# Kernel tuning notes

Hardware: AMD Instinct MI355X
Metric: run time of the kernel (lower is better)

The kernel has to match this reference:

```python
import jax, jax.numpy as jnp
import numpy as np

L = 32      # num_layer
N_ORD = 64  # order_of_a_LTImodel
U = 64      # u_size
Y = 64      # y_size
T = 8192    # sequence length
SCALE = 0.05  # keep block-bidiagonal A spectrally stable over 8192 steps


def setup_inputs() -> dict:
    key = jax.random.key(0)
    k_u, k_a, k_b0, k_bl, k_c = jax.random.split(key, 5)
    inp = {
        "input": jax.random.normal(k_u, (T, U), dtype=jnp.float32),
        # per-layer A_i weights (diagonal blocks)
        "A_stack": jax.random.normal(k_a, (L, N_ORD, N_ORD), dtype=jnp.float32) * SCALE,
        # layer-0 B (maps u -> state)
        "B0": jax.random.normal(k_b0, (N_ORD, U), dtype=jnp.float32) * SCALE,
        # layer i>=1 B weights (sub-diagonal coupling blocks)
        "B_lower": jax.random.normal(k_bl, (L - 1, N_ORD, N_ORD), dtype=jnp.float32) * SCALE,
        # per-layer C_i weights, concatenated along columns in forward
        "C_stack": jax.random.normal(k_c, (L, Y, N_ORD), dtype=jnp.float32),
        # D is frozen zeros (feedthrough=False)
        "D_w": jnp.zeros((Y, U), dtype=jnp.float32),
    }
    return inp


def _assemble(A_stack, B0, B_lower, C_stack):
    l, n, _ = A_stack.shape
    S = l * n
    A = jnp.zeros((S, S), A_stack.dtype)
    for i in range(l):  # fixed small structural loop
        A = A.at[i * n:(i + 1) * n, i * n:(i + 1) * n].set(A_stack[i])
    for i in range(1, l):
        A = A.at[i * n:(i + 1) * n, (i - 1) * n:i * n].set(B_lower[i - 1])
    B = jnp.concatenate([B0, jnp.zeros((S - n, B0.shape[1]), B0.dtype)], axis=0)
    # torch.cat([C_i], dim=1): [Y, L*n]
    C = jnp.transpose(C_stack, (1, 0, 2)).reshape(C_stack.shape[1], S)
    return A, B, C


def reference(input, A_stack, B0, B_lower, C_stack, D_w):
    A, B, C = _assemble(A_stack, B0, B_lower, C_stack)
    S = A.shape[0]
    x0 = jnp.zeros((S,), input.dtype)

    def step(x, u):
        y = C @ x + D_w @ u      # output BEFORE state update (y_t uses x_t)
        x_next = A @ x + B @ u
        return x_next, y

    _, ys = jax.lax.scan(step, x0, input)
    return ys  # [T, Y]
```

## Files before the change

### kernel.cpp

```cpp
#include <hip/hip_runtime.h>


#define LYR 32
#define NO  64
#define TSEQ 8192
#define PAD 32
#define PR2 (TSEQ+PAD)
#define PB2 ((size_t)PR2*NO)
#define KQ  2048

typedef _Float16 h16;
typedef _Float16 h16x8 __attribute__((ext_vector_type(8)));
typedef float    f32x4 __attribute__((ext_vector_type(4)));

#define MFMA16(a,b,c) __builtin_amdgcn_mfma_f32_16x16x32_f16((a),(b),(c),0,0,0)

__global__ __launch_bounds__(256) void prep_build(
    const float* __restrict__ u, const float* __restrict__ B0,
    const float* __restrict__ Bl, const float* __restrict__ Cst,
    const float* __restrict__ Ast,
    h16* __restrict__ xq, h16* __restrict__ ccast,
    h16* __restrict__ SN, h16* __restrict__ ST,
    h16* __restrict__ ktq, float* __restrict__ Dacc)
{
    __shared__ __align__(16) h16   Ah[64*72];
    __shared__ __align__(16) h16   kT[64*72];
    __shared__ __align__(16) float kf[64*68];
    const int tid = threadIdx.x;

    if (blockIdx.x < 32) {
        const int layer = blockIdx.x;
        const bool wantST = (layer & 3) == 0;
        const float* k0 = (layer == 0) ? B0 : (Bl + (size_t)(layer-1)*4096);
        const float* Aw = Ast + (size_t)layer*4096;
        for (int e8 = tid; e8 < 512; e8 += 256) {
            int n = e8 >> 3, m0 = (e8 & 7) << 3;
            f32x4 a0 = *(const f32x4*)&Aw[n*64 + m0];
            f32x4 a1 = *(const f32x4*)&Aw[n*64 + m0 + 4];
            h16 ah[8];
            #pragma unroll
            for (int t = 0; t < 4; t++) { ah[t] = (h16)a0[t]; ah[4+t] = (h16)a1[t]; }
            *(int4*)&Ah[n*72 + m0] = *(int4*)&ah[0];
            f32x4 b0 = *(const f32x4*)&k0[n*64 + m0];
            f32x4 b1 = *(const f32x4*)&k0[n*64 + m0 + 4];
            *(f32x4*)&kf[n*68 + m0]     = b0;
            *(f32x4*)&kf[n*68 + m0 + 4] = b1;
        }
        __syncthreads();

        const int wv = tid >> 6, lane = tid & 63, r = lane & 15, q = lane >> 4;
        const h16x8 a0 = *(const h16x8*)&Ah[(wv*16 + r)*72 + q*8];
        const h16x8 a1 = *(const h16x8*)&Ah[(wv*16 + r)*72 + 32 + q*8];

        for (int j = 0; j < 16; j++) {
            if (j > 0) {
                f32x4 acc[4] = {};
                #pragma unroll
                for (int c = 0; c < 4; c++) {
                    h16x8 b0 = *(const h16x8*)&kT[(c*16 + r)*72 + q*8];
                    h16x8 b1 = *(const h16x8*)&kT[(c*16 + r)*72 + 32 + q*8];
                    acc[c] = MFMA16(a0, b0, acc[c]);
                    acc[c] = MFMA16(a1, b1, acc[c]);
                }
                #pragma unroll
                for (int c = 0; c < 4; c++)
                    #pragma unroll
                    for (int g4 = 0; g4 < 4; g4++)
                        kf[(wv*16 + q*4 + g4)*68 + c*16 + r] = acc[c][g4];
                __syncthreads();
            }
            size_t base = (size_t)(layer*16 + j)*4096;
            for (int e8 = tid; e8 < 512; e8 += 256) {
                int n = e8 >> 3, m0 = (e8 & 7) << 3;
                f32x4 v0 = *(const f32x4*)&kf[n*68 + m0];
                f32x4 v1 = *(const f32x4*)&kf[n*68 + m0 + 4];
                h16 o[8];
                #pragma unroll
                for (int t = 0; t < 4; t++) { o[t] = (h16)v0[t]; o[4+t] = (h16)v1[t]; }
                if (!wantST)
                    *(int4*)&SN[base + (size_t)n*64 + m0] = *(int4*)&o[0];
                #pragma unroll
                for (int t = 0; t < 8; t++)
                    kT[(m0 + t)*72 + n] = o[t];
                if (wantST) {
                    h16 o2[8];
                    #pragma unroll
                    for (int t = 0; t < 8; t++) o2[t] = (h16)kf[(m0 + t)*68 + n];
                    *(int4*)&ST[base + (size_t)n*64 + m0] = *(int4*)&o2[0];
                }
            }
            __syncthreads();
        }
        return;
    }

    const int s1 = 256;
    const int s2 = 65536;
    const int s3 = 1792;
    const int s4 = 16384;
    const int s5 = 131072;
    const int s6 = 262144;
    const int total = s1+s2+s3+s4+s5+s6;
    const int4 z4 = make_int4(0,0,0,0);
    for (int e0 = (blockIdx.x - 32)*256 + tid; e0 < total; e0 += 512*256) {
        int e = e0;
        if (e < s1) { *(int4*)&xq[e*8] = z4; continue; }
        e -= s1;
        if (e < s2) {
            int el = e*8;
            f32x4 f0 = *(const f32x4*)&u[el];
            f32x4 f1 = *(const f32x4*)&u[el+4];
            h16 ov[8];
            #pragma unroll
            for (int j = 0; j < 4; j++) { ov[j] = (h16)f0[j]; ov[4+j] = (h16)f1[j]; }
            *(int4*)&xq[PAD*NO + el] = *(int4*)&ov[0];
            continue;
        }
        e -= s2;
        if (e < s3) {
            int b = e >> 8, off = (e & 255)*8;
            *(int4*)&xq[(size_t)(b+1)*PB2 + off] = z4;
            continue;
        }
        e -= s3;
        if (e < s4) {
            int el = e*8;
            f32x4 f0 = *(const f32x4*)&Cst[el];
            f32x4 f1 = *(const f32x4*)&Cst[el+4];
            h16 ov[8];
            #pragma unroll
            for (int j = 0; j < 4; j++) { ov[j] = (h16)f0[j]; ov[4+j] = (h16)f1[j]; }
            *(int4*)&ccast[el] = *(int4*)&ov[0];
            continue;
        }
        e -= s4;
        if (e < s5) { *(int4*)&ktq[e*8] = z4; continue; }
        e -= s5;
        *(int4*)&Dacc[e*4] = z4;
    }
}

__device__ __forceinline__ void comp_mm(const h16* __restrict__ X,
                                        const h16* __restrict__ Y,
                                        int wv, int r, int q, f32x4 acc[4])
{
    h16x8 a0 = *(const h16x8*)(X + (wv*16 + r)*64 + q*8);
    h16x8 a1 = *(const h16x8*)(X + (wv*16 + r)*64 + 32 + q*8);
    #pragma unroll
    for (int c = 0; c < 4; c++) {
        h16x8 b0 = *(const h16x8*)(Y + (c*16 + r)*64 + q*8);
        h16x8 b1 = *(const h16x8*)(Y + (c*16 + r)*64 + 32 + q*8);
        acc[c] = MFMA16(a0, b0, acc[c]);
        acc[c] = MFMA16(a1, b1, acc[c]);
    }
}

__global__ __launch_bounds__(256) void compose2(
    const h16* __restrict__ SN, const h16* __restrict__ ST,
    const h16* __restrict__ cc, h16* __restrict__ P2T,
    float* __restrict__ Dacc)
{
    const int tid = threadIdx.x, wv = tid>>6, lane = tid&63, r = lane&15, q = lane>>4;
    f32x4 acc[4] = {};
    int bid = blockIdx.x;
    if (bid < 248) {
        int g = bid / 31, m2 = bid % 31;
        int j0 = m2 > 15 ? m2 - 15 : 0;
        int j1 = m2 < 15 ? m2 : 15;
        const h16* X = SN + ((size_t)(4*g+1)*16 + j0)*4096;
        const h16* Y = ST + ((size_t)(4*g)*16 + (m2 - j0))*4096;
        for (int it = 0; it <= j1 - j0; ++it) {
            comp_mm(X, Y, wv, r, q, acc);
            X += 4096; Y -= 4096;
        }
        h16* o = P2T + ((size_t)g*31 + m2)*4096;
        #pragma unroll
        for (int c = 0; c < 4; c++)
            #pragma unroll
            for (int g4 = 0; g4 < 4; g4++)
                o[(c*16+r)*64 + wv*16 + q*4 + g4] = (h16)acc[c][g4];
    } else {
        int idx = bid - 248, g = idx >> 4, j = idx & 15;
        comp_mm(cc + (size_t)(4*g)*4096, ST + ((size_t)(4*g)*16 + j)*4096, wv, r, q, acc);
        float* Dd = Dacc + ((size_t)g*32 + j)*4096;
        #pragma unroll
        for (int c = 0; c < 4; c++)
            #pragma unroll
            for (int g4 = 0; g4 < 4; g4++)
                atomicAdd(&Dd[(wv*16 + q*4 + g4)*64 + c*16 + r], acc[c][g4]);
    }
}

__global__ __launch_bounds__(256) void compose3(
    const h16* __restrict__ SN, const h16* __restrict__ cc,
    const h16* __restrict__ P2T, h16* __restrict__ P3T,
    float* __restrict__ Dacc)
{
    const int tid = threadIdx.x, wv = tid>>6, lane = tid&63, r = lane&15, q = lane>>4;
    f32x4 acc[4] = {};
    int bid = blockIdx.x;
    if (bid < 240) {
        int g = bid / 30, m3 = bid % 30;
        int j1 = m3 < 15 ? m3 : 15;
        const h16* X = SN + ((size_t)(4*g+2)*16)*4096;
        const h16* Y = P2T + ((size_t)g*31 + m3)*4096;
        for (int it = 0; it <= j1; ++it) {
            comp_mm(X, Y, wv, r, q, acc);
            X += 4096; Y -= 4096;
        }
        h16* o = P3T + ((size_t)g*30 + m3)*4096;
        #pragma unroll
        for (int c = 0; c < 4; c++)
            #pragma unroll
            for (int g4 = 0; g4 < 4; g4++)
                o[(c*16+r)*64 + wv*16 + q*4 + g4] = (h16)acc[c][g4];
    } else {
        int idx = bid - 240, g = idx / 31, m2 = idx % 31;
        comp_mm(cc + (size_t)(4*g+1)*4096, P2T + ((size_t)g*31 + m2)*4096, wv, r, q, acc);
        float* Dd = Dacc + ((size_t)g*32 + m2 + 1)*4096;
        #pragma unroll
        for (int c = 0; c < 4; c++)
            #pragma unroll
            for (int g4 = 0; g4 < 4; g4++)
                atomicAdd(&Dd[(wv*16 + q*4 + g4)*64 + c*16 + r], acc[c][g4]);
    }
}

__global__ __launch_bounds__(256) void compose4(
    const h16* __restrict__ SN, const h16* __restrict__ cc,
    const h16* __restrict__ P3T, h16* __restrict__ ktq,
    float* __restrict__ Dacc)
{
    __shared__ h16 ldsT[64*72];
    const int tid = threadIdx.x, wv = tid>>6, lane = tid&63, r = lane&15, q = lane>>4;
    f32x4 acc[4] = {};
    int bid = blockIdx.x;
    if (bid < 232) {
        int g = bid / 29, m4 = bid % 29;
        int j1 = m4 < 15 ? m4 : 15;
        const h16* X = SN + ((size_t)(4*g+3)*16)*4096;
        const h16* Y = P3T + ((size_t)g*30 + m4)*4096;
        for (int it = 0; it <= j1; ++it) {
            comp_mm(X, Y, wv, r, q, acc);
            X += 4096; Y -= 4096;
        }
        h16* kq = ktq + (size_t)g*131072 + (size_t)(28 - m4)*64;
        #pragma unroll
        for (int c = 0; c < 4; c++)
            #pragma unroll
            for (int g4 = 0; g4 < 4; g4++) {
                h16 v = (h16)acc[c][g4];
                kq[(size_t)(wv*16 + q*4 + g4)*KQ + c*16 + r] = v;
                ldsT[(c*16+r)*72 + wv*16 + q*4 + g4] = v;
            }
        __syncthreads();
        f32x4 acc2[4] = {};
        const h16* Xc = cc + (size_t)(4*g+3)*4096;
        h16x8 a0 = *(const h16x8*)(Xc + (wv*16 + r)*64 + q*8);
        h16x8 a1 = *(const h16x8*)(Xc + (wv*16 + r)*64 + 32 + q*8);
        #pragma unroll
        for (int c = 0; c < 4; c++) {
            h16x8 b0 = *(const h16x8*)(&ldsT[(c*16+r)*72 + q*8]);
            h16x8 b1 = *(const h16x8*)(&ldsT[(c*16+r)*72 + 32 + q*8]);
            acc2[c] = MFMA16(a0, b0, acc2[c]);
            acc2[c] = MFMA16(a1, b1, acc2[c]);
        }
        float* Dd = Dacc + ((size_t)g*32 + m4 + 3)*4096;
        #pragma unroll
        for (int c = 0; c < 4; c++)
            #pragma unroll
            for (int g4 = 0; g4 < 4; g4++)
                atomicAdd(&Dd[(wv*16 + q*4 + g4)*64 + c*16 + r], acc2[c][g4]);
    } else {
        int idx = bid - 232, g = idx / 30, m3 = idx % 30;
        comp_mm(cc + (size_t)(4*g+2)*4096, P3T + ((size_t)g*30 + m3)*4096, wv, r, q, acc);
        float* Dd = Dacc + ((size_t)g*32 + m3 + 2)*4096;
        #pragma unroll
        for (int c = 0; c < 4; c++)
            #pragma unroll
            for (int g4 = 0; g4 < 4; g4++)
                atomicAdd(&Dd[(wv*16 + q*4 + g4)*64 + c*16 + r], acc[c][g4]);
    }
}

__global__ __launch_bounds__(256) void castD(const float* __restrict__ Dacc,
                                             h16* __restrict__ ktd)
{
    const int total4 = 8*32*4096/4;
    for (int idx4 = blockIdx.x*256 + threadIdx.x; idx4 < total4; idx4 += 256*256) {
        int idx = idx4 << 2;
        int gdo = idx >> 12;
        int g = gdo >> 5, dd = gdo & 31;
        int rem = idx & 4095;
        int y = rem >> 6, m = rem & 63;
        f32x4 f = *(const f32x4*)&Dacc[idx];
        h16 o4[4];
        #pragma unroll
        for (int t = 0; t < 4; t++) o4[t] = (h16)f[t];
        *(int2*)&ktd[(size_t)g*131072 + (size_t)y*KQ + (31 - dd)*64 + m] = *(int2*)&o4[0];
    }
}

template<int WRST>
__global__ __launch_bounds__(512) void stage(
    const h16* __restrict__ pin, h16* __restrict__ pout,
    const h16* __restrict__ ktqg, const h16* __restrict__ ktdg,
    float* __restrict__ out, int first)
{
    __shared__ __align__(16) h16   win[96*72];
    __shared__ __align__(16) float red[4*32*68];
    const int tid = threadIdx.x;
    const size_t t0 = (size_t)blockIdx.x * 64;

    for (int e = tid; e < 96*8; e += 512) {
        int rr = e >> 3, cc = e & 7;
        *(int4*)&win[rr*72 + cc*8] = *(const int4*)&pin[(t0 + rr)*64 + cc*8];
    }
    __syncthreads();

    const int wv = tid >> 6, lane = tid & 63, r = lane & 15, q = lane >> 4;
    const int half = wv >> 2, kq = wv & 3;
    const bool active = WRST || (half == 1);
    f32x4 acc[2][2][4] = {};
    if (active) {
        const h16* kb = half ? ktdg : ktqg;
        const h16* abase = &win[(r + kq*8)*72 + q*8];
        const h16* bbase = kb + (size_t)r*KQ + kq*512 + q*8;
#define LDA(st, s, ls) (*(const h16x8*)(abase + ((st)*32 + (s)*16 + ((ls)>>1))*72 + ((ls)&1)*32))
#define LDB(c, ls) (*(const h16x8*)(bbase + (size_t)(c)*(16*KQ) + (ls)*32))
        h16x8 a[2][2][2], b[2][4];
        #pragma unroll
        for (int sl = 0; sl < 2; sl++) {
            #pragma unroll
            for (int st = 0; st < 2; st++)
                #pragma unroll
                for (int s = 0; s < 2; s++) a[sl][st][s] = LDA(st, s, sl);
            #pragma unroll
            for (int c = 0; c < 4; c++) b[sl][c] = LDB(c, sl);
        }
        #pragma unroll
        for (int ls = 0; ls < 16; ls++) {
            h16x8 ca[2][2], cb[4];
            #pragma unroll
            for (int st = 0; st < 2; st++)
                #pragma unroll
                for (int s = 0; s < 2; s++) ca[st][s] = a[ls&1][st][s];
            #pragma unroll
            for (int c = 0; c < 4; c++) cb[c] = b[ls&1][c];
            if (ls < 14) {
                #pragma unroll
                for (int st = 0; st < 2; st++)
                    #pragma unroll
                    for (int s = 0; s < 2; s++) a[ls&1][st][s] = LDA(st, s, ls+2);
                #pragma unroll
                for (int c = 0; c < 4; c++) b[ls&1][c] = LDB(c, ls+2);
            }
            #pragma unroll
            for (int st = 0; st < 2; st++)
                #pragma unroll
                for (int s = 0; s < 2; s++)
                    #pragma unroll
                    for (int c = 0; c < 4; c++)
                        acc[st][s][c] = MFMA16(ca[st][s], cb[c], acc[st][s][c]);
        }
#undef LDA
#undef LDB
    }

    const int rh = half * (2*32*68);
    #pragma unroll
    for (int st = 0; st < 2; st++) {
        __syncthreads();
        if (active && kq >= 2) {
            float* myred = red + rh + (kq-2)*(32*68);
            #pragma unroll
            for (int s2 = 0; s2 < 2; s2++)
                #pragma unroll
                for (int c = 0; c < 4; c++)
                    #pragma unroll
                    for (int g4 = 0; g4 < 4; g4++)
                        myred[(s2*16 + q*4 + g4)*68 + c*16 + r] = acc[st][s2][c][g4];
        }
        __syncthreads();
        if (active && kq < 2) {
            float* myred = red + rh + kq*(32*68);
            #pragma unroll
            for (int s2 = 0; s2 < 2; s2++)
                #pragma unroll
                for (int c = 0; c < 4; c++)
                    #pragma unroll
                    for (int g4 = 0; g4 < 4; g4++)
                        myred[(s2*16 + q*4 + g4)*68 + c*16 + r] += acc[st][s2][c][g4];
        }
        __syncthreads();
        if (WRST && tid < 256) {
            int orow = tid >> 3, cb2 = (tid & 7) << 3;
            f32x4 u0 = *(const f32x4*)&red[orow*68 + cb2];
            f32x4 u1 = *(const f32x4*)&red[orow*68 + cb2 + 4];
            f32x4 v0 = *(const f32x4*)&red[32*68 + orow*68 + cb2];
            f32x4 v1 = *(const f32x4*)&red[32*68 + orow*68 + cb2 + 4];
            u0 += v0; u1 += v1;
            h16 ov[8];
            #pragma unroll
            for (int j = 0; j < 4; j++) { ov[j] = (h16)u0[j]; ov[4+j] = (h16)u1[j]; }
            *(int4*)&pout[(PAD + t0 + st*32 + orow)*64 + cb2] = *(int4*)&ov[0];
        }
        if (tid >= 256) {
            int t2 = tid - 256;
            int orow = t2 >> 3, cb2 = (t2 & 7) << 3;
            const float* base = red + 2*32*68;
            f32x4 u0 = *(const f32x4*)&base[orow*68 + cb2];
            f32x4 u1 = *(const f32x4*)&base[orow*68 + cb2 + 4];
            f32x4 v0 = *(const f32x4*)&base[32*68 + orow*68 + cb2];
            f32x4 v1 = *(const f32x4*)&base[32*68 + orow*68 + cb2 + 4];
            u0 += v0; u1 += v1;
            float* op = out + (t0 + st*32 + orow)*64 + cb2;
            if (first) {
                *(f32x4*)op = u0; *(f32x4*)(op+4) = u1;
            } else {
                f32x4 o0 = *(f32x4*)op, o1 = *(f32x4*)(op+4);
                o0 += u0; o1 += u1;
                *(f32x4*)op = o0; *(f32x4*)(op+4) = o1;
            }
        }
    }
}

extern "C" void kernel_launch(void* const* d_in, const int* in_sizes, int n_in,
                              void* d_out, int out_size, void* d_ws, size_t ws_size,
                              hipStream_t stream)
{
    const float* u   = (const float*)d_in[0];
    const float* Ast = (const float*)d_in[1];
    const float* B0  = (const float*)d_in[2];
    const float* Bl  = (const float*)d_in[3];
    const float* Cst = (const float*)d_in[4];
    float* out = (float*)d_out;
    (void)in_sizes; (void)n_in; (void)out_size; (void)ws_size;

    char* ws = (char*)d_ws;
    h16*   xq    = (h16*)ws;
    h16*   ccast = (h16*)(ws + 8421376);
    h16*   SN    = (h16*)(ws + 8683520);
    h16*   ST    = (h16*)(ws + 12877824);
    h16*   P2T   = (h16*)(ws + 17072128);
    h16*   P3T   = (h16*)(ws + 19103744);
    h16*   ktq   = (h16*)(ws + 21069824);
    h16*   ktd   = (h16*)(ws + 23166976);
    float* Dacc  = (float*)(ws + 25264128);

    prep_build<<<544, 256, 0, stream>>>(u, B0, Bl, Cst, Ast, xq, ccast, SN, ST, ktq, Dacc);
    compose2<<<376, 256, 0, stream>>>(SN, ST, ccast, P2T, Dacc);
    compose3<<<488, 256, 0, stream>>>(SN, ccast, P2T, P3T, Dacc);
    compose4<<<472, 256, 0, stream>>>(SN, ccast, P3T, ktq, Dacc);
    castD<<<256, 256, 0, stream>>>(Dacc, ktd);
    for (int g = 0; g < 7; g++) {
        stage<1><<<TSEQ/64, 512, 0, stream>>>(xq + (size_t)g*PB2, xq + (size_t)(g+1)*PB2,
                                              ktq + (size_t)g*131072, ktd + (size_t)g*131072,
                                              out, g == 0);
    }
    stage<0><<<TSEQ/64, 512, 0, stream>>>(xq + (size_t)7*PB2, xq,
                                          ktq + (size_t)7*131072, ktd + (size_t)7*131072,
                                          out, 0);
}
```

Baseline: 303.0 us.

## Compose layer-group kernels to 8-layer groups, halving sequential stage launches

Adds a compose5 pass that convolves pairs of 4-layer impulse-response blocks into 8-layer kernels (ktq8/ktd8). The sequential stage chain across the sequence then runs 4 launches instead of 8. Padding and window sizes are adjusted for the longer composed kernels. The goal is to cut serialized stage passes and reloads of intermediate state, at the cost of extra composition work and more fp16 rounding through the deeper products.

```diff
diff --git a/kernel.cpp b/kernel.cpp
--- a/kernel.cpp
+++ b/kernel.cpp
@@ -1,19 +1,20 @@
 #include <hip/hip_runtime.h>
 
 
-#define LYR 32
-#define NO  64
+#define NO   64
 #define TSEQ 8192
-#define PAD 32
-#define PR2 (TSEQ+PAD)
-#define PB2 ((size_t)PR2*NO)
-#define KQ  2048
+#define PAD8 40
+#define PRX  8240
+#define PBX  ((size_t)PRX*NO)
+#define KQ   2048
 
 typedef _Float16 h16;
 typedef _Float16 h16x8 __attribute__((ext_vector_type(8)));
 typedef float    f32x4 __attribute__((ext_vector_type(4)));
 
 #define MFMA16(a,b,c) __builtin_amdgcn_mfma_f32_16x16x32_f16((a),(b),(c),0,0,0)
+#define IMAX(a,b) ((a)>(b)?(a):(b))
+#define IMIN(a,b) ((a)<(b)?(a):(b))
 
 __global__ __launch_bounds__(256) void prep_build(
     const float* __restrict__ u, const float* __restrict__ B0,
@@ -21,7 +22,7 @@
     const float* __restrict__ Ast,
     h16* __restrict__ xq, h16* __restrict__ ccast,
     h16* __restrict__ SN, h16* __restrict__ ST,
-    h16* __restrict__ ktq, float* __restrict__ Dacc)
+    float* __restrict__ Dacc)
 {
     __shared__ __align__(16) h16   Ah[64*72];
     __shared__ __align__(16) h16   kT[64*72];
@@ -41,17 +42,13 @@
             #pragma unroll
             for (int t = 0; t < 4; t++) { ah[t] = (h16)a0[t]; ah[4+t] = (h16)a1[t]; }
             *(int4*)&Ah[n*72 + m0] = *(int4*)&ah[0];
-            f32x4 b0 = *(const f32x4*)&k0[n*64 + m0];
-            f32x4 b1 = *(const f32x4*)&k0[n*64 + m0 + 4];
-            *(f32x4*)&kf[n*68 + m0]     = b0;
-            *(f32x4*)&kf[n*68 + m0 + 4] = b1;
+            *(f32x4*)&kf[n*68 + m0]     = *(const f32x4*)&k0[n*64 + m0];
+            *(f32x4*)&kf[n*68 + m0 + 4] = *(const f32x4*)&k0[n*64 + m0 + 4];
         }
         __syncthreads();
-
         const int wv = tid >> 6, lane = tid & 63, r = lane & 15, q = lane >> 4;
         const h16x8 a0 = *(const h16x8*)&Ah[(wv*16 + r)*72 + q*8];
         const h16x8 a1 = *(const h16x8*)&Ah[(wv*16 + r)*72 + 32 + q*8];
-
         for (int j = 0; j < 16; j++) {
             if (j > 0) {
                 f32x4 acc[4] = {};
@@ -94,13 +91,12 @@
         return;
     }
 
-    const int s1 = 256;
+    const int s1 = 320;
     const int s2 = 65536;
-    const int s3 = 1792;
+    const int s3 = 960;
     const int s4 = 16384;
-    const int s5 = 131072;
     const int s6 = 262144;
-    const int total = s1+s2+s3+s4+s5+s6;
+    const int total = s1+s2+s3+s4+s6;
     const int4 z4 = make_int4(0,0,0,0);
     for (int e0 = (blockIdx.x - 32)*256 + tid; e0 < total; e0 += 512*256) {
         int e = e0;
@@ -113,13 +109,13 @@
             h16 ov[8];
             #pragma unroll
             for (int j = 0; j < 4; j++) { ov[j] = (h16)f0[j]; ov[4+j] = (h16)f1[j]; }
-            *(int4*)&xq[PAD*NO + el] = *(int4*)&ov[0];
+            *(int4*)&xq[PAD8*NO + el] = *(int4*)&ov[0];
             continue;
         }
         e -= s2;
         if (e < s3) {
-            int b = e >> 8, off = (e & 255)*8;
-            *(int4*)&xq[(size_t)(b+1)*PB2 + off] = z4;
+            int b = e / 320, off = (e % 320)*8;
+            *(int4*)&xq[(size_t)(b+1)*PBX + off] = z4;
             continue;
         }
         e -= s3;
@@ -134,8 +130,6 @@
             continue;
         }
         e -= s4;
-        if (e < s5) { *(int4*)&ktq[e*8] = z4; continue; }
-        e -= s5;
         *(int4*)&Dacc[e*4] = z4;
     }
 }
@@ -154,6 +148,30 @@
         acc[c] = MFMA16(a1, b1, acc[c]);
     }
 }
+__device__ __forceinline__ void conv_loop(const h16* X, const h16* Y, int n,
+                                          int wv, int r, int q, f32x4 acc[4])
+{
+    for (int it = 0; it < n; ++it) {
+        comp_mm(X, Y, wv, r, q, acc);
+        X += 4096; Y -= 4096;
+    }
+}
+__device__ __forceinline__ void write_N(h16* o, int wv, int r, int q, const f32x4 acc[4])
+{
+    #pragma unroll
+    for (int c = 0; c < 4; c++)
+        #pragma unroll
+        for (int g4 = 0; g4 < 4; g4++)
+            o[(size_t)(wv*16 + q*4 + g4)*64 + c*16 + r] = (h16)acc[c][g4];
+}
+__device__ __forceinline__ void write_T(h16* o, int wv, int r, int q, const f32x4 acc[4])
+{
+    #pragma unroll
+    for (int c = 0; c < 4; c++)
+        #pragma unroll
+        for (int g4 = 0; g4 < 4; g4++)
+            o[(size_t)(c*16 + r)*64 + wv*16 + q*4 + g4] = (h16)acc[c][g4];
+}
 
 __global__ __launch_bounds__(256) void compose2(
     const h16* __restrict__ SN, const h16* __restrict__ ST,
@@ -165,24 +183,15 @@
     int bid = blockIdx.x;
     if (bid < 248) {
         int g = bid / 31, m2 = bid % 31;
-        int j0 = m2 > 15 ? m2 - 15 : 0;
-        int j1 = m2 < 15 ? m2 : 15;
-        const h16* X = SN + ((size_t)(4*g+1)*16 + j0)*4096;
-        const h16* Y = ST + ((size_t)(4*g)*16 + (m2 - j0))*4096;
-        for (int it = 0; it <= j1 - j0; ++it) {
-            comp_mm(X, Y, wv, r, q, acc);
-            X += 4096; Y -= 4096;
-        }
-        h16* o = P2T + ((size_t)g*31 + m2)*4096;
-        #pragma unroll
-        for (int c = 0; c < 4; c++)
-            #pragma unroll
-            for (int g4 = 0; g4 < 4; g4++)
-                o[(c*16+r)*64 + wv*16 + q*4 + g4] = (h16)acc[c][g4];
+        int j0 = IMAX(0, m2 - 15);
+        int j1 = IMIN(15, m2);
+        conv_loop(SN + ((size_t)((4*g+1)*16) + j0)*4096,
+                  ST + ((size_t)((4*g)*16) + (m2 - j0))*4096, j1-j0+1, wv, r, q, acc);
+        write_T(P2T + ((size_t)(g*31 + m2))*4096, wv, r, q, acc);
     } else {
         int idx = bid - 248, g = idx >> 4, j = idx & 15;
-        comp_mm(cc + (size_t)(4*g)*4096, ST + ((size_t)(4*g)*16 + j)*4096, wv, r, q, acc);
-        float* Dd = Dacc + ((size_t)g*32 + j)*4096;
+        comp_mm(cc + (size_t)(4*g)*4096, ST + ((size_t)((4*g)*16) + j)*4096, wv, r, q, acc);
+        float* Dd = Dacc + ((size_t)(g*32 + j))*4096;
         #pragma unroll
         for (int c = 0; c < 4; c++)
             #pragma unroll
@@ -201,23 +210,14 @@
     int bid = blockIdx.x;
     if (bid < 240) {
         int g = bid / 30, m3 = bid % 30;
-        int j1 = m3 < 15 ? m3 : 15;
-        const h16* X = SN + ((size_t)(4*g+2)*16)*4096;
-        const h16* Y = P2T + ((size_t)g*31 + m3)*4096;
-        for (int it = 0; it <= j1; ++it) {
-            comp_mm(X, Y, wv, r, q, acc);
-            X += 4096; Y -= 4096;
-        }
-        h16* o = P3T + ((size_t)g*30 + m3)*4096;
-        #pragma unroll
-        for (int c = 0; c < 4; c++)
-            #pragma unroll
-            for (int g4 = 0; g4 < 4; g4++)
-                o[(c*16+r)*64 + wv*16 + q*4 + g4] = (h16)acc[c][g4];
+        int j1 = IMIN(15, m3);
+        conv_loop(SN + ((size_t)((4*g+2)*16))*4096,
+                  P2T + ((size_t)(g*31 + m3))*4096, j1+1, wv, r, q, acc);
+        write_T(P3T + ((size_t)(g*30 + m3))*4096, wv, r, q, acc);
     } else {
         int idx = bid - 240, g = idx / 31, m2 = idx % 31;
-        comp_mm(cc + (size_t)(4*g+1)*4096, P2T + ((size_t)g*31 + m2)*4096, wv, r, q, acc);
-        float* Dd = Dacc + ((size_t)g*32 + m2 + 1)*4096;
+        comp_mm(cc + (size_t)(4*g+1)*4096, P2T + ((size_t)(g*31 + m2))*4096, wv, r, q, acc);
+        float* Dd = Dacc + ((size_t)(g*32 + m2 + 1))*4096;
         #pragma unroll
         for (int c = 0; c < 4; c++)
             #pragma unroll
@@ -228,7 +228,8 @@
 
 __global__ __launch_bounds__(256) void compose4(
     const h16* __restrict__ SN, const h16* __restrict__ cc,
-    const h16* __restrict__ P3T, h16* __restrict__ ktq,
+    const h16* __restrict__ P3T,
+    h16* __restrict__ P4N, h16* __restrict__ P4T,
     float* __restrict__ Dacc)
 {
     __shared__ h16 ldsT[64*72];
@@ -237,22 +238,16 @@
     int bid = blockIdx.x;
     if (bid < 232) {
         int g = bid / 29, m4 = bid % 29;
-        int j1 = m4 < 15 ? m4 : 15;
-        const h16* X = SN + ((size_t)(4*g+3)*16)*4096;
-        const h16* Y = P3T + ((size_t)g*30 + m4)*4096;
-        for (int it = 0; it <= j1; ++it) {
-            comp_mm(X, Y, wv, r, q, acc);
-            X += 4096; Y -= 4096;
-        }
-        h16* kq = ktq + (size_t)g*131072 + (size_t)(28 - m4)*64;
-        #pragma unroll
-        for (int c = 0; c < 4; c++)
-            #pragma unroll
-            for (int g4 = 0; g4 < 4; g4++) {
-                h16 v = (h16)acc[c][g4];
-                kq[(size_t)(wv*16 + q*4 + g4)*KQ + c*16 + r] = v;
-                ldsT[(c*16+r)*72 + wv*16 + q*4 + g4] = v;
-            }
+        int j1 = IMIN(15, m4);
+        conv_loop(SN + ((size_t)((4*g+3)*16))*4096,
+                  P3T + ((size_t)(g*30 + m4))*4096, j1+1, wv, r, q, acc);
+        write_N(P4N + ((size_t)(g*29 + m4))*4096, wv, r, q, acc);
+        write_T(P4T + ((size_t)(g*29 + m4))*4096, wv, r, q, acc);
+        #pragma unroll
+        for (int c = 0; c < 4; c++)
+            #pragma unroll
+            for (int g4 = 0; g4 < 4; g4++)
+                ldsT[(c*16+r)*72 + wv*16 + q*4 + g4] = (h16)acc[c][g4];
         __syncthreads();
         f32x4 acc2[4] = {};
         const h16* Xc = cc + (size_t)(4*g+3)*4096;
@@ -265,7 +260,7 @@
             acc2[c] = MFMA16(a0, b0, acc2[c]);
             acc2[c] = MFMA16(a1, b1, acc2[c]);
         }
-        float* Dd = Dacc + ((size_t)g*32 + m4 + 3)*4096;
+        float* Dd = Dacc + ((size_t)(g*32 + m4 + 3))*4096;
         #pragma unroll
         for (int c = 0; c < 4; c++)
             #pragma unroll
@@ -273,8 +268,8 @@
                 atomicAdd(&Dd[(wv*16 + q*4 + g4)*64 + c*16 + r], acc2[c][g4]);
     } else {
         int idx = bid - 232, g = idx / 30, m3 = idx % 30;
-        comp_mm(cc + (size_t)(4*g+2)*4096, P3T + ((size_t)g*30 + m3)*4096, wv, r, q, acc);
-        float* Dd = Dacc + ((size_t)g*32 + m3 + 2)*4096;
+        comp_mm(cc + (size_t)(4*g+2)*4096, P3T + ((size_t)(g*30 + m3))*4096, wv, r, q, acc);
+        float* Dd = Dacc + ((size_t)(g*32 + m3 + 2))*4096;
         #pragma unroll
         for (int c = 0; c < 4; c++)
             #pragma unroll
@@ -284,37 +279,73 @@
 }
 
 __global__ __launch_bounds__(256) void castD(const float* __restrict__ Dacc,
-                                             h16* __restrict__ ktd)
+                                             h16* __restrict__ D4N)
 {
     const int total4 = 8*32*4096/4;
     for (int idx4 = blockIdx.x*256 + threadIdx.x; idx4 < total4; idx4 += 256*256) {
         int idx = idx4 << 2;
-        int gdo = idx >> 12;
-        int g = gdo >> 5, dd = gdo & 31;
-        int rem = idx & 4095;
-        int y = rem >> 6, m = rem & 63;
         f32x4 f = *(const f32x4*)&Dacc[idx];
         h16 o4[4];
         #pragma unroll
         for (int t = 0; t < 4; t++) o4[t] = (h16)f[t];
-        *(int2*)&ktd[(size_t)g*131072 + (size_t)y*KQ + (31 - dd)*64 + m] = *(int2*)&o4[0];
+        *(int2*)&D4N[idx] = *(int2*)&o4[0];
+    }
+}
+
+__global__ __launch_bounds__(256) void compose5(
+    const h16* __restrict__ P4N, const h16* __restrict__ P4T,
+    const h16* __restrict__ D4N, const float* __restrict__ D4F,
+    h16* __restrict__ ktq8, h16* __restrict__ ktd8)
+{
+    const int tid = threadIdx.x, wv = tid>>6, lane = tid&63, r = lane&15, q = lane>>4;
+    f32x4 acc[4] = {};
+    int bid = blockIdx.x;
+    if (bid < 128) {
+        int o = bid >> 5, m = bid & 31, D = m + 8;
+        int j0 = IMAX(4, D-32), j1 = IMIN(32, D-4);
+        conv_loop(P4N + ((size_t)((2*o+1)*29) + (j0-4))*4096,
+                  P4T + ((size_t)((2*o)*29) + (D-j0-4))*4096, j1-j0+1, wv, r, q, acc);
+        h16* kq = ktq8 + (size_t)o*131072 + (size_t)(39 - D)*64;
+        #pragma unroll
+        for (int c = 0; c < 4; c++)
+            #pragma unroll
+            for (int g4 = 0; g4 < 4; g4++)
+                kq[(size_t)(wv*16 + q*4 + g4)*KQ + c*16 + r] = (h16)acc[c][g4];
+    } else {
+        int idx = bid - 128, o = idx >> 5, m = idx & 31, D = m + 1;
+        int n = D - 4;
+        if (n > 0)
+            conv_loop(D4N + ((size_t)((2*o+1)*32))*4096,
+                      P4T + ((size_t)((2*o)*29) + (D-1-4))*4096, n, wv, r, q, acc);
+        const float* DF = D4F + ((size_t)((2*o)*32 + D-1))*4096;
+        #pragma unroll
+        for (int c = 0; c < 4; c++)
+            #pragma unroll
+            for (int g4 = 0; g4 < 4; g4++)
+                acc[c][g4] += DF[(size_t)(wv*16 + q*4 + g4)*64 + c*16 + r];
+        h16* kd = ktd8 + (size_t)o*131072 + (size_t)(32 - D)*64;
+        #pragma unroll
+        for (int c = 0; c < 4; c++)
+            #pragma unroll
+            for (int g4 = 0; g4 < 4; g4++)
+                kd[(size_t)(wv*16 + q*4 + g4)*KQ + c*16 + r] = (h16)acc[c][g4];
     }
 }
 
 template<int WRST>
-__global__ __launch_bounds__(512) void stage(
+__global__ __launch_bounds__(512) void stage8(
     const h16* __restrict__ pin, h16* __restrict__ pout,
     const h16* __restrict__ ktqg, const h16* __restrict__ ktdg,
     float* __restrict__ out, int first)
 {
-    __shared__ __align__(16) h16   win[96*72];
+    __shared__ __align__(16) h16   win[104*72];
     __shared__ __align__(16) float red[4*32*68];
     const int tid = threadIdx.x;
     const size_t t0 = (size_t)blockIdx.x * 64;
 
-    for (int e = tid; e < 96*8; e += 512) {
+    for (int e = tid; e < 104*8; e += 512) {
         int rr = e >> 3, cc = e & 7;
-        *(int4*)&win[rr*72 + cc*8] = *(const int4*)&pin[(t0 + rr)*64 + cc*8];
+        *(int4*)&win[rr*72 + cc*8] = *(const int4*)&pin[(t0 + 1 + rr)*64 + cc*8];
     }
     __syncthreads();
 
@@ -324,7 +355,7 @@
     f32x4 acc[2][2][4] = {};
     if (active) {
         const h16* kb = half ? ktdg : ktqg;
-        const h16* abase = &win[(r + kq*8)*72 + q*8];
+        const h16* abase = &win[(r + kq*8 + (half ? 7 : 0))*72 + q*8];
         const h16* bbase = kb + (size_t)r*KQ + kq*512 + q*8;
 #define LDA(st, s, ls) (*(const h16x8*)(abase + ((st)*32 + (s)*16 + ((ls)>>1))*72 + ((ls)&1)*32))
 #define LDB(c, ls) (*(const h16x8*)(bbase + (size_t)(c)*(16*KQ) + (ls)*32))
@@ -403,7 +434,7 @@
             h16 ov[8];
             #pragma unroll
             for (int j = 0; j < 4; j++) { ov[j] = (h16)u0[j]; ov[4+j] = (h16)u1[j]; }
-            *(int4*)&pout[(PAD + t0 + st*32 + orow)*64 + cb2] = *(int4*)&ov[0];
+            *(int4*)&pout[(PAD8 + t0 + st*32 + orow)*64 + cb2] = *(int4*)&ov[0];
         }
         if (tid >= 256) {
             int t2 = tid - 256;
@@ -439,27 +470,31 @@
     (void)in_sizes; (void)n_in; (void)out_size; (void)ws_size;
 
     char* ws = (char*)d_ws;
-    h16*   xq    = (h16*)ws;
-    h16*   ccast = (h16*)(ws + 8421376);
-    h16*   SN    = (h16*)(ws + 8683520);
-    h16*   ST    = (h16*)(ws + 12877824);
-    h16*   P2T   = (h16*)(ws + 17072128);
-    h16*   P3T   = (h16*)(ws + 19103744);
-    h16*   ktq   = (h16*)(ws + 21069824);
-    h16*   ktd   = (h16*)(ws + 23166976);
-    float* Dacc  = (float*)(ws + 25264128);
-
-    prep_build<<<544, 256, 0, stream>>>(u, B0, Bl, Cst, Ast, xq, ccast, SN, ST, ktq, Dacc);
+    h16*   xq   = (h16*)  (ws + 0);
+    h16*   ccast= (h16*)  (ws + 4218880);
+    h16*   SN   = (h16*)  (ws + 4481024);
+    h16*   ST   = (h16*)  (ws + 8675328);
+    h16*   P2T  = (h16*)  (ws + 12869632);
+    h16*   P3T  = (h16*)  (ws + 14901248);
+    h16*   P4N  = (h16*)  (ws + 16867328);
+    h16*   P4T  = (h16*)  (ws + 18767872);
+    float* Dacc = (float*)(ws + 20668416);
+    h16*   D4N  = (h16*)  (ws + 24862720);
+    h16*   ktq8 = (h16*)  (ws + 26959872);
+    h16*   ktd8 = (h16*)  (ws + 28008448);
+
+    prep_build<<<544, 256, 0, stream>>>(u, B0, Bl, Cst, Ast, xq, ccast, SN, ST, Dacc);
     compose2<<<376, 256, 0, stream>>>(SN, ST, ccast, P2T, Dacc);
     compose3<<<488, 256, 0, stream>>>(SN, ccast, P2T, P3T, Dacc);
-    compose4<<<472, 256, 0, stream>>>(SN, ccast, P3T, ktq, Dacc);
-    castD<<<256, 256, 0, stream>>>(Dacc, ktd);
-    for (int g = 0; g < 7; g++) {
-        stage<1><<<TSEQ/64, 512, 0, stream>>>(xq + (size_t)g*PB2, xq + (size_t)(g+1)*PB2,
-                                              ktq + (size_t)g*131072, ktd + (size_t)g*131072,
-                                              out, g == 0);
-    }
-    stage<0><<<TSEQ/64, 512, 0, stream>>>(xq + (size_t)7*PB2, xq,
-                                          ktq + (size_t)7*131072, ktd + (size_t)7*131072,
-                                          out, 0);
-}
+    compose4<<<472, 256, 0, stream>>>(SN, ccast, P3T, P4N, P4T, Dacc);
+    castD<<<256, 256, 0, stream>>>(Dacc, D4N);
+    compose5<<<256, 256, 0, stream>>>(P4N, P4T, D4N, Dacc, ktq8, ktd8);
+    for (int g = 0; g < 3; g++) {
+        stage8<1><<<TSEQ/64, 512, 0, stream>>>(xq + (size_t)g*PBX, xq + (size_t)(g+1)*PBX,
+                                               ktq8 + (size_t)g*131072, ktd8 + (size_t)g*131072,
+                                               out, g == 0);
+    }
+    stage8<0><<<TSEQ/64, 512, 0, stream>>>(xq + (size_t)3*PBX, xq,
+                                           ktq8 + (size_t)3*131072, ktd8 + (size_t)3*131072,
+                                           out, 0);
+}
```

After: 262.8 us. 13.3% less time.
